# Optimization experiments

Hardware: AMD Instinct MI355X
Metric: run time of the kernel (lower is better)

## Reference

```python
import jax, jax.numpy as jnp
import numpy as np
import math

EMBED_DIM = 1024
NUM_HEADS = 16
HEAD_DIM = EMBED_DIM // NUM_HEADS
SCALING = HEAD_DIM ** -0.5
SOFTPLUS_BETA = math.log(2.0)


def linear(x, W, b):
    # torch nn.Linear: x @ W.T + b
    return jnp.einsum('...i,oi->...o', x, W) + b


def efficient_causal_attention_parallel(x, y, z):
    # x: (B, n, d1), y: (B, n, d1), z: (B, n, d2)
    n = x.shape[1]
    # outer products per step, then causal prefix-sum over n
    accum = jnp.cumsum(jnp.einsum('bni,bnj->bnij', y, z), axis=1)  # (B, n, d1, d2)
    res = jnp.einsum('bni,bnij->bnj', x, accum)                    # (B, n, d2)
    length_div = jnp.arange(1, n + 1, dtype=x.dtype)[None, :, None]
    return res / length_div


def setup_inputs() -> dict:
    key = jax.random.key(0)
    ks = jax.random.split(key, 12)
    tgt_len, bsz, plen = 2048, 2, 32
    E = EMBED_DIM
    s = 1.0 / math.sqrt(E)
    return {
        'query': jax.random.normal(ks[0], (tgt_len, bsz, E), jnp.float32),
        'pquery': jax.random.normal(ks[1], (plen, bsz, E), jnp.float32),
        'Wpq': jax.random.normal(ks[2], (E, E), jnp.float32) * s,
        'bpq': jnp.zeros((E,), jnp.float32),
        'Wq': jax.random.normal(ks[3], (E, E), jnp.float32) * s,
        'bq': jnp.zeros((E,), jnp.float32),
        'Wpc': jax.random.normal(ks[4], (E, E), jnp.float32) * s,
        'bpc': jnp.zeros((E,), jnp.float32),
        'Wc': jax.random.normal(ks[5], (E, E), jnp.float32) * s,
        'bc': jnp.zeros((E,), jnp.float32),
        'Wo': jax.random.normal(ks[6], (E, E), jnp.float32) * s,
        'bo': jnp.zeros((E,), jnp.float32),
    }


def reference(query, pquery, Wpq, bpq, Wq, bq, Wpc, bpc, Wc, bc, Wo, bo):
    tgt_len, bsz, E = query.shape
    plen = pquery.shape[0]
    H, D = NUM_HEADS, HEAD_DIM
    BH = bsz * H

    # pq: (plen, bsz, E) -> (bsz, H, plen, D), scaled
    pq = linear(pquery, Wpq, bpq).reshape(plen, bsz, H, D)
    pq = jnp.transpose(pq, (1, 2, 0, 3)) * SCALING

    # _compute_pattention: k (BH, tgt_len, D) @ pq^T (BH, D, plen)
    kp = linear(query, Wpc, bpc).reshape(tgt_len, BH, D).transpose(1, 0, 2)
    pqm = pq.reshape(BH, plen, D).transpose(0, 2, 1)  # (BH, D, plen)
    pattn = jnp.matmul(kp, pqm)                        # (BH, tgt_len, plen)
    pattn = jax.nn.softplus(SOFTPLUS_BETA * pattn) / SOFTPLUS_BETA

    q = (linear(query, Wq, bq) * SCALING).reshape(tgt_len, BH, D).transpose(1, 0, 2)
    kv = linear(query, Wc, bc).reshape(tgt_len, BH, D).transpose(1, 0, 2)  # tied k=v

    attn_weights = efficient_causal_attention_parallel(q, kv, pattn)  # (BH, tgt_len, plen)
    attn_weights = jax.nn.softmax(attn_weights, axis=-1)
    attn = efficient_causal_attention_parallel(attn_weights, pattn, kv)  # (BH, tgt_len, D)

    attn = attn.transpose(1, 0, 2).reshape(tgt_len, bsz, E)
    return linear(attn, Wo, bo)
```

## Files before the change

### kernel.cpp

```cpp
#include <hip/hip_runtime.h>
#include <hip/hip_bf16.h>
#include <math.h>

typedef __hip_bfloat16 bf16;
typedef __attribute__((ext_vector_type(8))) short bf16x8;
typedef __attribute__((ext_vector_type(4))) float f32x4;

__device__ __forceinline__ short f2bf_s(float v){ union{ bf16 b; short s;} u; u.b = __float2bfloat16(v); return u.s; }

__device__ __forceinline__ void gl_lds16(const bf16* g, short* l) {
    __builtin_amdgcn_global_load_lds(
        (const __attribute__((address_space(1))) void*)g,
        (__attribute__((address_space(3))) void*)l, 16, 0, 0);
}

#define LN2F 0.69314718055994531f

__device__ __forceinline__ void cvt_store4(bf16* d, size_t idx, float4 v) {
    union { ushort4 u; bf16 b[4]; } o;
    o.b[0] = __float2bfloat16(v.x);
    o.b[1] = __float2bfloat16(v.y);
    o.b[2] = __float2bfloat16(v.z);
    o.b[3] = __float2bfloat16(v.w);
    ((ushort4*)d)[idx] = o.u;
}

__device__ __forceinline__ void st_out(float* p, float v){ *p = v; }
__device__ __forceinline__ void st_out(bf16* p, float v){ *p = __float2bfloat16(v); }

__global__ __launch_bounds__(256)
void conv1_kernel(const float* __restrict__ query, const float* __restrict__ pquery,
                  const float* __restrict__ Wpq, bf16* __restrict__ qbf,
                  bf16* __restrict__ pqy, bf16* __restrict__ wpq)
{
    int blk = blockIdx.x;
    const float* s; bf16* d; int i;
    if (blk < 4096)      { s = query;  d = qbf; i = blk * 256 + threadIdx.x; }
    else if (blk < 4160) { s = pquery; d = pqy; i = (blk - 4096) * 256 + threadIdx.x; }
    else                 { s = Wpq;    d = wpq; i = (blk - 4160) * 256 + threadIdx.x; }
    cvt_store4(d, i, ((const float4*)s)[i]);
}

__global__ __launch_bounds__(256)
void conv2_kernel(const float* __restrict__ Wpc, const float* __restrict__ Wq,
                  const float* __restrict__ Wc, const float* __restrict__ Wo,
                  const float* __restrict__ bpc, const float* __restrict__ bq,
                  const float* __restrict__ bc,
                  bf16* __restrict__ wcat, bf16* __restrict__ wo_bf,
                  float* __restrict__ biascat)
{
    int blk = blockIdx.x;
    if (blk < 3072) {
        const float* s = (blk < 1024) ? Wpc : ((blk < 2048) ? Wq : Wc);
        int rel = (blk & 1023) * 256 + threadIdx.x;
        bf16* d = wcat + (size_t)(blk >> 10) * 1048576;
        cvt_store4(d, rel, ((const float4*)s)[rel]);
    } else if (blk < 4096) {
        int rel = (blk - 3072) * 256 + threadIdx.x;
        cvt_store4(wo_bf, rel, ((const float4*)Wo)[rel]);
    } else {
        int i = (blk - 4096) * 256 + threadIdx.x;
        float v = (i < 1024) ? bpc[i] : ((i < 2048) ? bq[i - 1024] : bc[i - 2048]);
        biascat[i] = v;
    }
}

template<typename TO>
__global__ __launch_bounds__(256)
void gemm_bf16_nt(const bf16* __restrict__ A, const bf16* __restrict__ B,
                  const float* __restrict__ bias, TO* __restrict__ C,
                  int M, int N, int K, float scale_all, float scale_mid)
{
    __shared__ short As[128 * 32];
    __shared__ short Bs[128 * 32];

    const int tid  = threadIdx.x;
    const int lane = tid & 63;
    const int wave = tid >> 6;
    const int m0 = blockIdx.y * 128;
    const int n0 = blockIdx.x * 128;
    const int wm = (wave >> 1) * 64;
    const int wn = (wave & 1) * 64;

    f32x4 acc[4][4] = {};

    const int c0 = tid, c1 = tid + 256;
    const int r0 = c0 >> 2, s0 = c0 & 3;
    const int r1 = c1 >> 2, s1 = c1 & 3;

    const int kb = lane >> 4;
    const int rr = lane & 15;

    for (int k0 = 0; k0 < K; k0 += 32) {
        __syncthreads();
        gl_lds16(A + (size_t)(m0 + r0) * K + k0 + s0 * 8, As + c0 * 8);
        gl_lds16(A + (size_t)(m0 + r1) * K + k0 + s1 * 8, As + c1 * 8);
        gl_lds16(B + (size_t)(n0 + r0) * K + k0 + s0 * 8, Bs + c0 * 8);
        gl_lds16(B + (size_t)(n0 + r1) * K + k0 + s1 * 8, Bs + c1 * 8);
        __syncthreads();

        bf16x8 af[4], bfr[4];
        #pragma unroll
        for (int mi = 0; mi < 4; ++mi)
            af[mi] = *(const bf16x8*)(As + (wm + mi * 16 + rr) * 32 + kb * 8);
        #pragma unroll
        for (int ni = 0; ni < 4; ++ni)
            bfr[ni] = *(const bf16x8*)(Bs + (wn + ni * 16 + rr) * 32 + kb * 8);
        #pragma unroll
        for (int mi = 0; mi < 4; ++mi)
            #pragma unroll
            for (int ni = 0; ni < 4; ++ni)
                acc[mi][ni] = __builtin_amdgcn_mfma_f32_16x16x32_bf16(
                    af[mi], bfr[ni], acc[mi][ni], 0, 0, 0);
    }

    const int col_l = lane & 15;
    const int row_q = lane >> 4;
    #pragma unroll
    for (int ni = 0; ni < 4; ++ni) {
        int col = n0 + wn + ni * 16 + col_l;
        float bb = bias[col];
        float sc = ((col >> 10) == 1) ? scale_mid : scale_all;
        #pragma unroll
        for (int mi = 0; mi < 4; ++mi) {
            #pragma unroll
            for (int r = 0; r < 4; ++r) {
                int row = m0 + wm + mi * 16 + row_q * 4 + r;
                st_out(C + (size_t)row * N + col, sc * (acc[mi][ni][r] + bb));
            }
        }
    }
}

__global__ __launch_bounds__(256)
void gemm_pq_partial(const bf16* __restrict__ A, const bf16* __restrict__ B,
                     float* __restrict__ part)
{
    __shared__ short As[64 * 32];
    __shared__ short Bs[128 * 32];

    const int tid  = threadIdx.x;
    const int lane = tid & 63;
    const int wave = tid >> 6;
    const int n0 = blockIdx.x * 128;
    const int kslice = blockIdx.y;
    const int kbase = kslice * 128;

    f32x4 acc[4][2] = {};

    const int ra = tid >> 2, sa = tid & 3;
    const int c0 = tid, c1 = tid + 256;
    const int rb0 = c0 >> 2, sb0 = c0 & 3;
    const int rb1 = c1 >> 2, sb1 = c1 & 3;

    const int kb = lane >> 4;
    const int rr = lane & 15;

    for (int k0 = kbase; k0 < kbase + 128; k0 += 32) {
        __syncthreads();
        gl_lds16(A + (size_t)ra * 1024 + k0 + sa * 8, As + tid * 8);
        gl_lds16(B + (size_t)(n0 + rb0) * 1024 + k0 + sb0 * 8, Bs + c0 * 8);
        gl_lds16(B + (size_t)(n0 + rb1) * 1024 + k0 + sb1 * 8, Bs + c1 * 8);
        __syncthreads();

        bf16x8 af[4], bfr[2];
        #pragma unroll
        for (int mi = 0; mi < 4; ++mi)
            af[mi] = *(const bf16x8*)(As + (mi * 16 + rr) * 32 + kb * 8);
        #pragma unroll
        for (int ni = 0; ni < 2; ++ni)
            bfr[ni] = *(const bf16x8*)(Bs + (wave * 32 + ni * 16 + rr) * 32 + kb * 8);
        #pragma unroll
        for (int mi = 0; mi < 4; ++mi)
            #pragma unroll
            for (int ni = 0; ni < 2; ++ni)
                acc[mi][ni] = __builtin_amdgcn_mfma_f32_16x16x32_bf16(
                    af[mi], bfr[ni], acc[mi][ni], 0, 0, 0);
    }

    const int col_l = lane & 15;
    const int row_q = lane >> 4;
    float* dst = part + (size_t)kslice * 65536;
    #pragma unroll
    for (int ni = 0; ni < 2; ++ni) {
        int col = n0 + wave * 32 + ni * 16 + col_l;
        #pragma unroll
        for (int mi = 0; mi < 4; ++mi) {
            #pragma unroll
            for (int r = 0; r < 4; ++r) {
                int row = mi * 16 + row_q * 4 + r;
                dst[(size_t)row * 1024 + col] = acc[mi][ni][r];
            }
        }
    }
}

__global__ __launch_bounds__(256)
void pq_reduce(const float* __restrict__ part, const float* __restrict__ bias,
               bf16* __restrict__ pq)
{
    int gid = blockIdx.x * 256 + threadIdx.x;
    int n = gid & 1023;
    float s = bias[n];
    #pragma unroll
    for (int k = 0; k < 8; ++k) s += part[(size_t)k * 65536 + gid];
    pq[gid] = __float2bfloat16(0.125f * s);
}

__global__ __launch_bounds__(256)
void pattn_sum_kernel(const bf16* __restrict__ kp, const bf16* __restrict__ kv,
                      const bf16* __restrict__ pqb, bf16* __restrict__ pattn,
                      float* __restrict__ Sbuf, int T, int ld)
{
    __shared__ short sKP[64 * 72];
    __shared__ short sKVT[64 * 72];
    __shared__ short sPQ[32 * 72];
    __shared__ short sPT[32 * 72];

    const int c = blockIdx.x, bh = blockIdx.y;
    const int b = bh >> 4, h = bh & 15;
    const int t0 = c * 64;
    const int tid = threadIdx.x;
    const int lane = tid & 63, wave = tid >> 6;
    const int rr = lane & 15, kb = lane >> 4;
    const int m0w = wave * 16;

    #pragma unroll
    for (int l = 0; l < 2; ++l) {
        int idx = tid + l * 256;
        int t = idx >> 3, d8 = (idx & 7) * 8;
        size_t g = (size_t)((t0 + t) * 2 + b) * ld + h * 64 + d8;
        uint4 vk = *(const uint4*)(kp + g);
        *(uint4*)(sKP + t * 72 + d8) = vk;
        uint4 vv = *(const uint4*)(kv + g + 2048);
        union { uint4 u; short s[8]; } cw; cw.u = vv;
        #pragma unroll
        for (int i = 0; i < 8; ++i) sKVT[(d8 + i) * 72 + t] = cw.s[i];
    }
    {
        int p = tid >> 3, d8 = (tid & 7) * 8;
        uint4 v = *(const uint4*)(pqb + (size_t)(p * 2 + b) * 1024 + h * 64 + d8);
        *(uint4*)(sPQ + p * 72 + d8) = v;
    }
    __syncthreads();

    {
        bf16x8 a0 = *(const bf16x8*)(sKP + (m0w + rr) * 72 + kb * 8);
        bf16x8 a1 = *(const bf16x8*)(sKP + (m0w + rr) * 72 + 32 + kb * 8);
        f32x4 acc[2] = {};
        #pragma unroll
        for (int nt = 0; nt < 2; ++nt) {
            bf16x8 b0 = *(const bf16x8*)(sPQ + (nt * 16 + rr) * 72 + kb * 8);
            bf16x8 b1 = *(const bf16x8*)(sPQ + (nt * 16 + rr) * 72 + 32 + kb * 8);
            acc[nt] = __builtin_amdgcn_mfma_f32_16x16x32_bf16(a0, b0, acc[nt], 0, 0, 0);
            acc[nt] = __builtin_amdgcn_mfma_f32_16x16x32_bf16(a1, b1, acc[nt], 0, 0, 0);
        }
        #pragma unroll
        for (int nt = 0; nt < 2; ++nt)
            #pragma unroll
            for (int r = 0; r < 4; ++r) {
                int t = m0w + kb * 4 + r;
                int p = nt * 16 + rr;
                float z = LN2F * acc[nt][r];
                float sp = (fmaxf(z, 0.f) + log1pf(__expf(-fabsf(z)))) / LN2F;
                short sb = f2bf_s(sp);
                sPT[p * 72 + t] = sb;
                ((unsigned short*)pattn)[((size_t)bh * T + t0 + t) * 32 + p] = (unsigned short)sb;
            }
    }
    __syncthreads();

    {
        bf16x8 a0 = *(const bf16x8*)(sKVT + (m0w + rr) * 72 + kb * 8);
        bf16x8 a1 = *(const bf16x8*)(sKVT + (m0w + rr) * 72 + 32 + kb * 8);
        f32x4 acc[2] = {};
        #pragma unroll
        for (int nt = 0; nt < 2; ++nt) {
            bf16x8 b0 = *(const bf16x8*)(sPT + (nt * 16 + rr) * 72 + kb * 8);
            bf16x8 b1 = *(const bf16x8*)(sPT + (nt * 16 + rr) * 72 + 32 + kb * 8);
            acc[nt] = __builtin_amdgcn_mfma_f32_16x16x32_bf16(a0, b0, acc[nt], 0, 0, 0);
            acc[nt] = __builtin_amdgcn_mfma_f32_16x16x32_bf16(a1, b1, acc[nt], 0, 0, 0);
        }
        float* Sdst = Sbuf + ((size_t)bh * 32 + c) * 2048;
        #pragma unroll
        for (int nt = 0; nt < 2; ++nt)
            #pragma unroll
            for (int r = 0; r < 4; ++r) {
                int i = m0w + kb * 4 + r;
                int j = nt * 16 + rr;
                Sdst[i * 32 + j] = acc[nt][r];
            }
    }
}

__global__ __launch_bounds__(256)
void prefix_state_kernel(float* __restrict__ Sbuf)
{
    const int NCH = 32;
    int gid = blockIdx.x * 256 + threadIdx.x;
    int bh = gid >> 11, e = gid & 2047;
    float* p = Sbuf + (size_t)bh * NCH * 2048 + e;
    float run = 0.f;
    #pragma unroll
    for (int c = 0; c < NCH; ++c) {
        float t = p[c * 2048];
        p[c * 2048] = run;
        run += t;
    }
}

__global__ __launch_bounds__(256)
void chunk_attn(const bf16* __restrict__ qg, const bf16* __restrict__ kvg,
                const bf16* __restrict__ pg, const float* __restrict__ Sg,
                bf16* __restrict__ attn, int T, int ld)
{
    __shared__ short sm[30720];
    short* sQ   = sm;
    short* sKV  = sm + 4608;
    short* sKVT = sm + 9216;
    short* sW   = sm + 13824;
    short* sAW  = sm + 18432;
    short* sS   = sm + 20992;
    short* sST  = sm + 23552;
    short* sP   = sm + 25856;
    short* sPT  = sm + 28416;

    const int bh = blockIdx.y, c = blockIdx.x;
    const int b = bh >> 4, h = bh & 15;
    const int t0 = c * 64;
    const int tid = threadIdx.x;
    const int lane = tid & 63;
    const int wave = tid >> 6;
    const int rr = lane & 15;
    const int kb = lane >> 4;
    const int m0w = wave * 16;
    const float* Sblk = Sg + ((size_t)bh * 32 + c) * 2048;

    #pragma unroll
    for (int l = 0; l < 2; ++l) {
        int idx = tid + l * 256;
        int t = idx >> 3, d8 = (idx & 7) * 8;
        size_t g = (size_t)((t0 + t) * 2 + b) * ld + h * 64 + d8;
        uint4 qv = *(const uint4*)(qg + g);
        *(uint4*)(sQ + t * 72 + d8) = qv;
        uint4 kvv = *(const uint4*)(kvg + g);
        *(uint4*)(sKV + t * 72 + d8) = kvv;
        union { uint4 u; short s[8]; } ck; ck.u = kvv;
        #pragma unroll
        for (int i = 0; i < 8; ++i) sKVT[(d8 + i) * 72 + t] = ck.s[i];
    }
    {
        int t = tid >> 2, j8 = (tid & 3) * 8;
        uint4 pv = *(const uint4*)(pg + ((size_t)bh * T + t0 + t) * 32 + j8);
        *(uint4*)(sP + t * 40 + j8) = pv;
        union { uint4 u; short s[8]; } cp; cp.u = pv;
        #pragma unroll
        for (int i = 0; i < 8; ++i) sPT[(j8 + i) * 72 + t] = cp.s[i];

        float4 s0 = *(const float4*)(Sblk + t * 32 + j8);
        float4 s1 = *(const float4*)(Sblk + t * 32 + j8 + 4);
        union { ushort4 u; short s[4]; bf16 bb[4]; } c0, c1;
        c0.bb[0] = __float2bfloat16(s0.x);
        c0.bb[1] = __float2bfloat16(s0.y);
        c0.bb[2] = __float2bfloat16(s0.z);
        c0.bb[3] = __float2bfloat16(s0.w);
        c1.bb[0] = __float2bfloat16(s1.x);
        c1.bb[1] = __float2bfloat16(s1.y);
        c1.bb[2] = __float2bfloat16(s1.z);
        c1.bb[3] = __float2bfloat16(s1.w);
        *(ushort4*)(sS + t * 40 + j8) = c0.u;
        *(ushort4*)(sS + t * 40 + j8 + 4) = c1.u;
        #pragma unroll
        for (int i = 0; i < 4; ++i) sST[(j8 + i) * 72 + t] = c0.s[i];
        #pragma unroll
        for (int i = 0; i < 4; ++i) sST[(j8 + 4 + i) * 72 + t] = c1.s[i];
    }
    __syncthreads();

    {
        bf16x8 aq0 = *(const bf16x8*)(sQ + (m0w + rr) * 72 + kb * 8);
        bf16x8 aq1 = *(const bf16x8*)(sQ + (m0w + rr) * 72 + 32 + kb * 8);
        f32x4 acc[4] = {};
        #pragma unroll
        for (int nt = 0; nt < 4; ++nt) {
            bf16x8 b0 = *(const bf16x8*)(sKV + (nt * 16 + rr) * 72 + kb * 8);
            bf16x8 b1 = *(const bf16x8*)(sKV + (nt * 16 + rr) * 72 + 32 + kb * 8);
            acc[nt] = __builtin_amdgcn_mfma_f32_16x16x32_bf16(aq0, b0, acc[nt], 0, 0, 0);
            acc[nt] = __builtin_amdgcn_mfma_f32_16x16x32_bf16(aq1, b1, acc[nt], 0, 0, 0);
        }
        #pragma unroll
        for (int nt = 0; nt < 4; ++nt)
            #pragma unroll
            for (int r = 0; r < 4; ++r) {
                int t = m0w + kb * 4 + r;
                int s = nt * 16 + rr;
                sW[t * 72 + s] = f2bf_s((s <= t) ? acc[nt][r] : 0.f);
            }
    }
    __syncthreads();

    {
        bf16x8 aq0 = *(const bf16x8*)(sQ + (m0w + rr) * 72 + kb * 8);
        bf16x8 aq1 = *(const bf16x8*)(sQ + (m0w + rr) * 72 + 32 + kb * 8);
        bf16x8 aw0 = *(const bf16x8*)(sW + (m0w + rr) * 72 + kb * 8);
        bf16x8 aw1 = *(const bf16x8*)(sW + (m0w + rr) * 72 + 32 + kb * 8);
        f32x4 acc[2] = {};
        #pragma unroll
        for (int nt = 0; nt < 2; ++nt) {
            bf16x8 bs0 = *(const bf16x8*)(sST + (nt * 16 + rr) * 72 + kb * 8);
            bf16x8 bs1 = *(const bf16x8*)(sST + (nt * 16 + rr) * 72 + 32 + kb * 8);
            bf16x8 bp0 = *(const bf16x8*)(sPT + (nt * 16 + rr) * 72 + kb * 8);
            bf16x8 bp1 = *(const bf16x8*)(sPT + (nt * 16 + rr) * 72 + 32 + kb * 8);
            acc[nt] = __builtin_amdgcn_mfma_f32_16x16x32_bf16(aq0, bs0, acc[nt], 0, 0, 0);
            acc[nt] = __builtin_amdgcn_mfma_f32_16x16x32_bf16(aq1, bs1, acc[nt], 0, 0, 0);
            acc[nt] = __builtin_amdgcn_mfma_f32_16x16x32_bf16(aw0, bp0, acc[nt], 0, 0, 0);
            acc[nt] = __builtin_amdgcn_mfma_f32_16x16x32_bf16(aw1, bp1, acc[nt], 0, 0, 0);
        }
        #pragma unroll
        for (int r = 0; r < 4; ++r) {
            int t = m0w + kb * 4 + r;
            float inv_len = 1.0f / (float)(t0 + t + 1);
            float v0 = acc[0][r] * inv_len;
            float v1 = acc[1][r] * inv_len;
            float m = fmaxf(v0, v1);
            m = fmaxf(m, __shfl_xor(m, 1));
            m = fmaxf(m, __shfl_xor(m, 2));
            m = fmaxf(m, __shfl_xor(m, 4));
            m = fmaxf(m, __shfl_xor(m, 8));
            float e0 = __expf(v0 - m), e1 = __expf(v1 - m);
            float s = e0 + e1;
            s += __shfl_xor(s, 1);
            s += __shfl_xor(s, 2);
            s += __shfl_xor(s, 4);
            s += __shfl_xor(s, 8);
            float rs = 1.0f / s;
            sAW[t * 40 + rr]      = f2bf_s(e0 * rs);
            sAW[t * 40 + 16 + rr] = f2bf_s(e1 * rs);
        }
    }
    __syncthreads();

    {
        bf16x8 aa = *(const bf16x8*)(sAW + (m0w + rr) * 40 + kb * 8);
        f32x4 acc[4] = {};
        #pragma unroll
        for (int nt = 0; nt < 4; ++nt) {
            bf16x8 bp = *(const bf16x8*)(sP + (nt * 16 + rr) * 40 + kb * 8);
            acc[nt] = __builtin_amdgcn_mfma_f32_16x16x32_bf16(aa, bp, acc[nt], 0, 0, 0);
        }
        __syncthreads();
        #pragma unroll
        for (int nt = 0; nt < 4; ++nt)
            #pragma unroll
            for (int r = 0; r < 4; ++r) {
                int t = m0w + kb * 4 + r;
                int s = nt * 16 + rr;
                sW[t * 72 + s] = f2bf_s((s <= t) ? acc[nt][r] : 0.f);
            }
    }
    __syncthreads();

    {
        bf16x8 aa  = *(const bf16x8*)(sAW + (m0w + rr) * 40 + kb * 8);
        bf16x8 ap0 = *(const bf16x8*)(sW + (m0w + rr) * 72 + kb * 8);
        bf16x8 ap1 = *(const bf16x8*)(sW + (m0w + rr) * 72 + 32 + kb * 8);
        f32x4 acc[4] = {};
        #pragma unroll
        for (int nt = 0; nt < 4; ++nt) {
            bf16x8 bs = *(const bf16x8*)(sS + (nt * 16 + rr) * 40 + kb * 8);
            bf16x8 bk0 = *(const bf16x8*)(sKVT + (nt * 16 + rr) * 72 + kb * 8);
            bf16x8 bk1 = *(const bf16x8*)(sKVT + (nt * 16 + rr) * 72 + 32 + kb * 8);
            acc[nt] = __builtin_amdgcn_mfma_f32_16x16x32_bf16(aa,  bs,  acc[nt], 0, 0, 0);
            acc[nt] = __builtin_amdgcn_mfma_f32_16x16x32_bf16(ap0, bk0, acc[nt], 0, 0, 0);
            acc[nt] = __builtin_amdgcn_mfma_f32_16x16x32_bf16(ap1, bk1, acc[nt], 0, 0, 0);
        }
        #pragma unroll
        for (int nt = 0; nt < 4; ++nt)
            #pragma unroll
            for (int r = 0; r < 4; ++r) {
                int t = m0w + kb * 4 + r;
                int d = nt * 16 + rr;
                float v = acc[nt][r] / (float)(t0 + t + 1);
                ((unsigned short*)attn)[((size_t)((t0 + t) * 2 + b)) * 1024 + h * 64 + d] =
                    (unsigned short)f2bf_s(v);
            }
    }
}

extern "C" void kernel_launch(void* const* d_in, const int* in_sizes, int n_in,
                              void* d_out, int out_size, void* d_ws, size_t ws_size,
                              hipStream_t stream) {
    const float* query  = (const float*)d_in[0];
    const float* pquery = (const float*)d_in[1];
    const float* Wpq = (const float*)d_in[2];
    const float* bpq = (const float*)d_in[3];
    const float* Wq  = (const float*)d_in[4];
    const float* bq  = (const float*)d_in[5];
    const float* Wpc = (const float*)d_in[6];
    const float* bpc = (const float*)d_in[7];
    const float* Wc  = (const float*)d_in[8];
    const float* bc  = (const float*)d_in[9];
    const float* Wo  = (const float*)d_in[10];
    const float* bo  = (const float*)d_in[11];
    float* out = (float*)d_out;

    const int T = 2048, E = 1024, MROWS = 4096;
    const int NCH = 32;

    float* ws = (float*)d_ws;
    float* pq_f      = ws;
    float* Cbig_f    = pq_f + 65536;
    float* pattn_f   = Cbig_f + 6291456;
    float* S_buf     = pattn_f + 1048576;
    float* qbf_f     = S_buf + 2097152;
    float* wcat_f    = qbf_f + 2097152;
    float* wo_f      = wcat_f + 1572864;

    bf16* pq_bf   = (bf16*)pq_f;
    bf16* Cbig    = (bf16*)Cbig_f;
    bf16* pattn_bf= (bf16*)pattn_f;
    bf16* qbf     = (bf16*)qbf_f;
    bf16* wcat    = (bf16*)wcat_f;
    bf16* wpq_bf  = (bf16*)wcat_f;
    bf16* wo_bf   = (bf16*)wo_f;
    bf16* pqy_bf  = (bf16*)pattn_f;
    float* biascat = pattn_f + 32768;
    float* pq_part = S_buf;
    bf16* attn_bf = qbf;

    conv1_kernel<<<5184, 256, 0, stream>>>(query, pquery, Wpq, qbf, pqy_bf, wpq_bf);
    gemm_pq_partial<<<dim3(8, 8), 256, 0, stream>>>(pqy_bf, wpq_bf, pq_part);
    pq_reduce<<<256, 256, 0, stream>>>(pq_part, bpq, pq_bf);

    conv2_kernel<<<4108, 256, 0, stream>>>(Wpc, Wq, Wc, Wo, bpc, bq, bc, wcat, wo_bf, biascat);

    gemm_bf16_nt<bf16><<<dim3(24, 32), 256, 0, stream>>>(
        qbf, wcat, biascat, Cbig, MROWS, 3072, E, 1.0f, 0.125f);

    pattn_sum_kernel<<<dim3(NCH, 32), 256, 0, stream>>>(
        Cbig, Cbig, pq_bf, pattn_bf, S_buf, T, 3072);
    prefix_state_kernel<<<256, 256, 0, stream>>>(S_buf);
    chunk_attn<<<dim3(NCH, 32), 256, 0, stream>>>(
        Cbig + 1024, Cbig + 2048, pattn_bf, S_buf, attn_bf, T, 3072);
    gemm_bf16_nt<float><<<dim3(8, 32), 256, 0, stream>>>(
        attn_bf, wo_bf, bo, out, MROWS, E, E, 1.0f, 1.0f);
}
```

Measured before the change: 198.8 us.

## Merge conversion kernels, shrink chunk_attn LDS, use 64-row tiles for output GEMM

Merges the two fp32-to-bf16 conversion kernels into a single launch; to make that possible, Wpq now gets its own workspace buffer instead of aliasing wcat. The output projection GEMM switches to a 64x128 tile kernel, doubling the block count to 512 so more CUs are busy. chunk_attn now builds its transposed KV tile later, from LDS, reusing the Q buffer, which cuts shared memory per block and may raise occupancy. The trade-offs are a smaller per-block tile with less reuse in the output GEMM and an extra LDS pass in chunk_attn.

Measured after the change: 190.9 us. -4.0%, faster.

```diff
diff --git a/kernel.cpp b/kernel.cpp
--- a/kernel.cpp
+++ b/kernel.cpp
@@ -29,39 +29,40 @@
 __device__ __forceinline__ void st_out(bf16* p, float v){ *p = __float2bfloat16(v); }
 
 __global__ __launch_bounds__(256)
-void conv1_kernel(const float* __restrict__ query, const float* __restrict__ pquery,
-                  const float* __restrict__ Wpq, bf16* __restrict__ qbf,
-                  bf16* __restrict__ pqy, bf16* __restrict__ wpq)
+void conv_all(const float* __restrict__ query, const float* __restrict__ pquery,
+              const float* __restrict__ Wpq, const float* __restrict__ Wpc,
+              const float* __restrict__ Wq, const float* __restrict__ Wc,
+              const float* __restrict__ Wo,
+              const float* __restrict__ bpc, const float* __restrict__ bq,
+              const float* __restrict__ bc,
+              bf16* __restrict__ qbf, bf16* __restrict__ pqy, bf16* __restrict__ wpq,
+              bf16* __restrict__ wcat, bf16* __restrict__ wo_bf,
+              float* __restrict__ biascat)
 {
     int blk = blockIdx.x;
-    const float* s; bf16* d; int i;
-    if (blk < 4096)      { s = query;  d = qbf; i = blk * 256 + threadIdx.x; }
-    else if (blk < 4160) { s = pquery; d = pqy; i = (blk - 4096) * 256 + threadIdx.x; }
-    else                 { s = Wpq;    d = wpq; i = (blk - 4160) * 256 + threadIdx.x; }
-    cvt_store4(d, i, ((const float4*)s)[i]);
-}
-
-__global__ __launch_bounds__(256)
-void conv2_kernel(const float* __restrict__ Wpc, const float* __restrict__ Wq,
-                  const float* __restrict__ Wc, const float* __restrict__ Wo,
-                  const float* __restrict__ bpc, const float* __restrict__ bq,
-                  const float* __restrict__ bc,
-                  bf16* __restrict__ wcat, bf16* __restrict__ wo_bf,
-                  float* __restrict__ biascat)
-{
-    int blk = blockIdx.x;
-    if (blk < 3072) {
-        const float* s = (blk < 1024) ? Wpc : ((blk < 2048) ? Wq : Wc);
-        int rel = (blk & 1023) * 256 + threadIdx.x;
-        bf16* d = wcat + (size_t)(blk >> 10) * 1048576;
-        cvt_store4(d, rel, ((const float4*)s)[rel]);
-    } else if (blk < 4096) {
-        int rel = (blk - 3072) * 256 + threadIdx.x;
-        cvt_store4(wo_bf, rel, ((const float4*)Wo)[rel]);
+    if (blk < 4096) {
+        int i = blk * 256 + threadIdx.x;
+        cvt_store4(qbf, i, ((const float4*)query)[i]);
+    } else if (blk < 4160) {
+        int i = (blk - 4096) * 256 + threadIdx.x;
+        cvt_store4(pqy, i, ((const float4*)pquery)[i]);
+    } else if (blk < 5184) {
+        int i = (blk - 4160) * 256 + threadIdx.x;
+        cvt_store4(wpq, i, ((const float4*)Wpq)[i]);
+    } else if (blk < 8256) {
+        int rel = blk - 5184;
+        const float* s = (rel < 1024) ? Wpc : ((rel < 2048) ? Wq : Wc);
+        int i = (rel & 1023) * 256 + threadIdx.x;
+        cvt_store4(wcat + (size_t)(rel >> 10) * 1048576, i, ((const float4*)s)[i]);
+    } else if (blk < 9280) {
+        int i = (blk - 8256) * 256 + threadIdx.x;
+        cvt_store4(wo_bf, i, ((const float4*)Wo)[i]);
     } else {
-        int i = (blk - 4096) * 256 + threadIdx.x;
-        float v = (i < 1024) ? bpc[i] : ((i < 2048) ? bq[i - 1024] : bc[i - 2048]);
-        biascat[i] = v;
+        int i = (blk - 9280) * 256 + threadIdx.x;
+        if (i < 3072) {
+            float v = (i < 1024) ? bpc[i] : ((i < 2048) ? bq[i - 1024] : bc[i - 2048]);
+            biascat[i] = v;
+        }
     }
 }
 
@@ -127,6 +128,71 @@
             for (int r = 0; r < 4; ++r) {
                 int row = m0 + wm + mi * 16 + row_q * 4 + r;
                 st_out(C + (size_t)row * N + col, sc * (acc[mi][ni][r] + bb));
+            }
+        }
+    }
+}
+
+__global__ __launch_bounds__(256)
+void gemm_bf16_nt64(const bf16* __restrict__ A, const bf16* __restrict__ B,
+                    const float* __restrict__ bias, float* __restrict__ C,
+                    int M, int N, int K)
+{
+    __shared__ short As[64 * 32];
+    __shared__ short Bs[128 * 32];
+
+    const int tid  = threadIdx.x;
+    const int lane = tid & 63;
+    const int wave = tid >> 6;
+    const int m0 = blockIdx.y * 64;
+    const int n0 = blockIdx.x * 128;
+    const int wm = (wave >> 1) * 32;
+    const int wn = (wave & 1) * 64;
+
+    f32x4 acc[2][4] = {};
+
+    const int ra = tid >> 2, sa = tid & 3;
+    const int c0 = tid, c1 = tid + 256;
+    const int rb0 = c0 >> 2, sb0 = c0 & 3;
+    const int rb1 = c1 >> 2, sb1 = c1 & 3;
+
+    const int kb = lane >> 4;
+    const int rr = lane & 15;
+
+    for (int k0 = 0; k0 < K; k0 += 32) {
+        __syncthreads();
+        gl_lds16(A + (size_t)(m0 + ra) * K + k0 + sa * 8, As + tid * 8);
+        gl_lds16(B + (size_t)(n0 + rb0) * K + k0 + sb0 * 8, Bs + c0 * 8);
+        gl_lds16(B + (size_t)(n0 + rb1) * K + k0 + sb1 * 8, Bs + c1 * 8);
+        __syncthreads();
+
+        bf16x8 af[2], bfr[4];
+        #pragma unroll
+        for (int mi = 0; mi < 2; ++mi)
+            af[mi] = *(const bf16x8*)(As + (wm + mi * 16 + rr) * 32 + kb * 8);
+        #pragma unroll
+        for (int ni = 0; ni < 4; ++ni)
+            bfr[ni] = *(const bf16x8*)(Bs + (wn + ni * 16 + rr) * 32 + kb * 8);
+        #pragma unroll
+        for (int mi = 0; mi < 2; ++mi)
+            #pragma unroll
+            for (int ni = 0; ni < 4; ++ni)
+                acc[mi][ni] = __builtin_amdgcn_mfma_f32_16x16x32_bf16(
+                    af[mi], bfr[ni], acc[mi][ni], 0, 0, 0);
+    }
+
+    const int col_l = lane & 15;
+    const int row_q = lane >> 4;
+    #pragma unroll
+    for (int ni = 0; ni < 4; ++ni) {
+        int col = n0 + wn + ni * 16 + col_l;
+        float bb = bias[col];
+        #pragma unroll
+        for (int mi = 0; mi < 2; ++mi) {
+            #pragma unroll
+            for (int r = 0; r < 4; ++r) {
+                int row = m0 + wm + mi * 16 + row_q * 4 + r;
+                C[(size_t)row * N + col] = acc[mi][ni][r] + bb;
             }
         }
     }
@@ -314,16 +380,15 @@
                 const bf16* __restrict__ pg, const float* __restrict__ Sg,
                 bf16* __restrict__ attn, int T, int ld)
 {
-    __shared__ short sm[30720];
+    __shared__ short sm[26112];
     short* sQ   = sm;
     short* sKV  = sm + 4608;
-    short* sKVT = sm + 9216;
-    short* sW   = sm + 13824;
-    short* sAW  = sm + 18432;
-    short* sS   = sm + 20992;
-    short* sST  = sm + 23552;
-    short* sP   = sm + 25856;
-    short* sPT  = sm + 28416;
+    short* sW   = sm + 9216;
+    short* sAW  = sm + 13824;
+    short* sS   = sm + 16384;
+    short* sST  = sm + 18944;
+    short* sP   = sm + 21248;
+    short* sPT  = sm + 23808;
 
     const int bh = blockIdx.y, c = blockIdx.x;
     const int b = bh >> 4, h = bh & 15;
@@ -345,9 +410,6 @@
         *(uint4*)(sQ + t * 72 + d8) = qv;
         uint4 kvv = *(const uint4*)(kvg + g);
         *(uint4*)(sKV + t * 72 + d8) = kvv;
-        union { uint4 u; short s[8]; } ck; ck.u = kvv;
-        #pragma unroll
-        for (int i = 0; i < 8; ++i) sKVT[(d8 + i) * 72 + t] = ck.s[i];
     }
     {
         int t = tid >> 2, j8 = (tid & 3) * 8;
@@ -440,7 +502,17 @@
     }
     __syncthreads();
 
-    {
+    short* sKVT = sQ;
+    {
+        #pragma unroll
+        for (int l = 0; l < 2; ++l) {
+            int idx = tid + l * 256;
+            int t = idx >> 3, d8 = (idx & 7) * 8;
+            union { uint4 u; short s[8]; } ck;
+            ck.u = *(const uint4*)(sKV + t * 72 + d8);
+            #pragma unroll
+            for (int i = 0; i < 8; ++i) sKVT[(d8 + i) * 72 + t] = ck.s[i];
+        }
         bf16x8 aa = *(const bf16x8*)(sAW + (m0w + rr) * 40 + kb * 8);
         f32x4 acc[4] = {};
         #pragma unroll
@@ -515,24 +587,25 @@
     float* qbf_f     = S_buf + 2097152;
     float* wcat_f    = qbf_f + 2097152;
     float* wo_f      = wcat_f + 1572864;
+    float* wpq_f     = wo_f + 524288;
 
     bf16* pq_bf   = (bf16*)pq_f;
     bf16* Cbig    = (bf16*)Cbig_f;
     bf16* pattn_bf= (bf16*)pattn_f;
     bf16* qbf     = (bf16*)qbf_f;
     bf16* wcat    = (bf16*)wcat_f;
-    bf16* wpq_bf  = (bf16*)wcat_f;
     bf16* wo_bf   = (bf16*)wo_f;
+    bf16* wpq_bf  = (bf16*)wpq_f;
     bf16* pqy_bf  = (bf16*)pattn_f;
     float* biascat = pattn_f + 32768;
     float* pq_part = S_buf;
     bf16* attn_bf = qbf;
 
-    conv1_kernel<<<5184, 256, 0, stream>>>(query, pquery, Wpq, qbf, pqy_bf, wpq_bf);
+    conv_all<<<9292, 256, 0, stream>>>(query, pquery, Wpq, Wpc, Wq, Wc, Wo,
+                                       bpc, bq, bc, qbf, pqy_bf, wpq_bf,
+                                       wcat, wo_bf, biascat);
     gemm_pq_partial<<<dim3(8, 8), 256, 0, stream>>>(pqy_bf, wpq_bf, pq_part);
     pq_reduce<<<256, 256, 0, stream>>>(pq_part, bpq, pq_bf);
-
-    conv2_kernel<<<4108, 256, 0, stream>>>(Wpc, Wq, Wc, Wo, bpc, bq, bc, wcat, wo_bf, biascat);
 
     gemm_bf16_nt<bf16><<<dim3(24, 32), 256, 0, stream>>>(
         qbf, wcat, biascat, Cbig, MROWS, 3072, E, 1.0f, 0.125f);
@@ -542,6 +615,6 @@
     prefix_state_kernel<<<256, 256, 0, stream>>>(S_buf);
     chunk_attn<<<dim3(NCH, 32), 256, 0, stream>>>(
         Cbig + 1024, Cbig + 2048, pattn_bf, S_buf, attn_bf, T, 3072);
-    gemm_bf16_nt<float><<<dim3(8, 32), 256, 0, stream>>>(
-        attn_bf, wo_bf, bo, out, MROWS, E, E, 1.0f, 1.0f);
-}
+    gemm_bf16_nt64<<<dim3(8, 64), 256, 0, stream>>>(
+        attn_bf, wo_bf, bo, out, MROWS, E, E);
+}
```
